# Kernel tuning notes

Hardware: AMD Instinct MI355X
Metric: run time of the kernel (lower is better)

## Reference

```python
import jax, jax.numpy as jnp
import numpy as np

ACT = jax.nn.leaky_relu  # Decima uses leaky_relu activations


def _mlp(x, params):
    # Linear + act chain (activation applied after every layer, incl. last, as in the torch code)
    for W, b in params:
        x = ACT(x @ W + b)
    return x


def setup_inputs() -> dict:
    key = jax.random.key(0)
    N, E, D = 500_000, 4_000_000, 8  # nodes, edges per depth, max_depth
    ks = jax.random.split(key, 32)
    inp = {}
    inp["inputs"] = jax.random.normal(ks[0], (N, 5), dtype=jnp.float32)
    inp["adj_src"] = jax.random.randint(ks[1], (D, E), 0, N, dtype=jnp.int32)
    inp["adj_dst"] = jax.random.randint(ks[2], (D, E), 0, N, dtype=jnp.int32)
    inp["masks"] = (jax.random.uniform(ks[3], (D, N, 1)) > 0.5).astype(jnp.float32)
    # MLP stacks: prep 5->16->32->8, proc/agg 8->16->32->8 (xavier-ish init, zero bias)
    dims = {"prep": [(5, 16), (16, 32), (32, 8)],
            "proc": [(8, 16), (16, 32), (32, 8)],
            "agg": [(8, 16), (16, 32), (32, 8)]}
    i = 4
    for name, ds in dims.items():
        for j, (a, b) in enumerate(ds):
            scale = np.sqrt(6.0 / (a + b)).astype(np.float32)
            inp[f"{name}_W{j}"] = jax.random.uniform(ks[i], (a, b), jnp.float32, -scale, scale)
            inp[f"{name}_b{j}"] = jnp.zeros((b,), jnp.float32)
            i += 1
    return inp


def reference(inputs, adj_src, adj_dst, masks,
              prep_W0, prep_b0, prep_W1, prep_b1, prep_W2, prep_b2,
              proc_W0, proc_b0, proc_W1, proc_b1, proc_W2, proc_b2,
              agg_W0, agg_b0, agg_W1, agg_b1, agg_W2, agg_b2):
    prep = [(prep_W0, prep_b0), (prep_W1, prep_b1), (prep_W2, prep_b2)]
    proc = [(proc_W0, proc_b0), (proc_W1, proc_b1), (proc_W2, proc_b2)]
    agg = [(agg_W0, agg_b0), (agg_W1, agg_b1), (agg_W2, agg_b2)]
    N = inputs.shape[0]
    max_depth = adj_src.shape[0]

    x = _mlp(inputs, prep)  # [N, 8]
    for d in range(max_depth):  # small fixed loop over depths
        y = _mlp(x, proc)  # [N, 8]
        # sparse adj matmul (unit-valued adjacency): out[i] = sum_{j: (i,j) in adj} y[j]
        y = jax.ops.segment_sum(y[adj_src[d]], adj_dst[d], num_segments=N)
        y = _mlp(y, agg)
        x = x + y * masks[d]  # mask + residual
    return x
```

## Files before the change

### kernel.cpp

```cpp
#include <hip/hip_runtime.h>
#include <hip/hip_fp16.h>


typedef unsigned long long u64;
typedef unsigned int u32;
typedef int v4i __attribute__((ext_vector_type(4)));

#define BKT_BITS 10
#define BKT_SIZE 1024
#define MAXNB    512
#define NBLK     256

template <int CH> struct Cfg;
template <> struct Cfg<4> { static const int CAPC = 6;  static const int SUBC = 24; };
template <> struct Cfg<2> { static const int CAPC = 14; static const int SUBC = 32; };
template <> struct Cfg<1> { static const int CAPC = 30; static const int SUBC = 64; };

__device__ __forceinline__ float lrelu(float v) { return fmaxf(v, 0.01f * v); }

template <int IN>
__device__ __forceinline__ void mlp3(const float* __restrict__ xin, float* __restrict__ yout,
    const float* __restrict__ sW0, const float* __restrict__ sb0,
    const float* __restrict__ sW1, const float* __restrict__ sb1,
    const float* __restrict__ sW2, const float* __restrict__ sb2)
{
    float h1[16];
#pragma unroll
    for (int o = 0; o < 16; ++o) {
        float s = sb0[o];
#pragma unroll
        for (int a = 0; a < IN; ++a) s = fmaf(xin[a], sW0[a * 16 + o], s);
        h1[o] = lrelu(s);
    }
    float h2[32];
#pragma unroll
    for (int o = 0; o < 32; ++o) {
        float s = sb1[o];
#pragma unroll
        for (int a = 0; a < 16; ++a) s = fmaf(h1[a], sW1[a * 32 + o], s);
        h2[o] = lrelu(s);
    }
#pragma unroll
    for (int o = 0; o < 8; ++o) {
        float s = sb2[o];
#pragma unroll
        for (int a = 0; a < 32; ++a) s = fmaf(h2[a], sW2[a * 8 + o], s);
        yout[o] = lrelu(s);
    }
}

__device__ __forceinline__ void ldw(float* d, const float* s, int n) {
    for (int t = threadIdx.x; t < n; t += 256) d[t] = s[t];
}

__device__ __forceinline__ uint4 pack_h8(const float* y) {
    __half2 p0 = __floats2half2_rn(y[0], y[1]);
    __half2 p1 = __floats2half2_rn(y[2], y[3]);
    __half2 p2 = __floats2half2_rn(y[4], y[5]);
    __half2 p3 = __floats2half2_rn(y[6], y[7]);
    uint4 v;
    v.x = *(u32*)&p0; v.y = *(u32*)&p1; v.z = *(u32*)&p2; v.w = *(u32*)&p3;
    return v;
}

__global__ __launch_bounds__(256) void prep_proc_kernel(
    const float* __restrict__ in, float* __restrict__ x, uint4* __restrict__ y,
    const float* pW0, const float* pb0, const float* pW1, const float* pb1,
    const float* pW2, const float* pb2,
    const float* cW0, const float* cb0, const float* cW1, const float* cb1,
    const float* cW2, const float* cb2, int N)
{
    __shared__ float P0[80],  Pb0[16], P1[512], Pb1[32], P2[256], Pb2[8];
    __shared__ float C0[128], Cb0[16], C1[512], Cb1[32], C2[256], Cb2[8];
    ldw(P0, pW0, 80);  ldw(Pb0, pb0, 16); ldw(P1, pW1, 512); ldw(Pb1, pb1, 32);
    ldw(P2, pW2, 256); ldw(Pb2, pb2, 8);
    ldw(C0, cW0, 128); ldw(Cb0, cb0, 16); ldw(C1, cW1, 512); ldw(Cb1, cb1, 32);
    ldw(C2, cW2, 256); ldw(Cb2, cb2, 8);
    __syncthreads();
    int i = blockIdx.x * 256 + threadIdx.x;
    if (i >= N) return;
    float xin[5];
#pragma unroll
    for (int k = 0; k < 5; ++k) xin[k] = in[(size_t)i * 5 + k];
    float xv[8];
    mlp3<5>(xin, xv, P0, Pb0, P1, Pb1, P2, Pb2);
    float4* xp = (float4*)(x + 8 * (size_t)i);
    xp[0] = make_float4(xv[0], xv[1], xv[2], xv[3]);
    xp[1] = make_float4(xv[4], xv[5], xv[6], xv[7]);
    float yv[8];
    mlp3<8>(xv, yv, C0, Cb0, C1, Cb1, C2, Cb2);
    y[i] = pack_h8(yv);
}

template <bool DO_PROC, int CHUNKS>
__global__ __launch_bounds__(256) void aggproc_kernel(
    const uint4* __restrict__ acc, float* __restrict__ x, const float* __restrict__ mask,
    uint4* __restrict__ y,
    const float* aW0, const float* ab0, const float* aW1, const float* ab1,
    const float* aW2, const float* ab2,
    const float* cW0, const float* cb0, const float* cW1, const float* cb1,
    const float* cW2, const float* cb2, int N)
{
    __shared__ float A0[128], Ab0[16], A1[512], Ab1[32], A2[256], Ab2[8];
    __shared__ float C0[128], Cb0[16], C1[512], Cb1[32], C2[256], Cb2[8];
    ldw(A0, aW0, 128); ldw(Ab0, ab0, 16); ldw(A1, aW1, 512); ldw(Ab1, ab1, 32);
    ldw(A2, aW2, 256); ldw(Ab2, ab2, 8);
    if (DO_PROC) {
        ldw(C0, cW0, 128); ldw(Cb0, cb0, 16); ldw(C1, cW1, 512); ldw(Cb1, cb1, 32);
        ldw(C2, cW2, 256); ldw(Cb2, cb2, 8);
    }
    __syncthreads();
    int i = blockIdx.x * 256 + threadIdx.x;
    if (i >= N) return;
    float ain[8] = {0.f, 0.f, 0.f, 0.f, 0.f, 0.f, 0.f, 0.f};
#pragma unroll
    for (int c = 0; c < CHUNKS; ++c) {
        uint4 v = acc[(size_t)c * N + i];
        float2 f0 = __half22float2(*(__half2*)&v.x);
        float2 f1 = __half22float2(*(__half2*)&v.y);
        float2 f2 = __half22float2(*(__half2*)&v.z);
        float2 f3 = __half22float2(*(__half2*)&v.w);
        ain[0] += f0.x; ain[1] += f0.y; ain[2] += f1.x; ain[3] += f1.y;
        ain[4] += f2.x; ain[5] += f2.y; ain[6] += f3.x; ain[7] += f3.y;
    }
    float ya[8];
    mlp3<8>(ain, ya, A0, Ab0, A1, Ab1, A2, Ab2);
    float m = mask[i];
    float4* xp = (float4*)(x + 8 * (size_t)i);
    float4 x0 = xp[0], x1 = xp[1];
    float xn[8] = {x0.x + ya[0] * m, x0.y + ya[1] * m, x0.z + ya[2] * m, x0.w + ya[3] * m,
                   x1.x + ya[4] * m, x1.y + ya[5] * m, x1.z + ya[6] * m, x1.w + ya[7] * m};
    xp[0] = make_float4(xn[0], xn[1], xn[2], xn[3]);
    xp[1] = make_float4(xn[4], xn[5], xn[6], xn[7]);
    if (DO_PROC) {
        float yv[8];
        mlp3<8>(xn, yv, C0, Cb0, C1, Cb1, C2, Cb2);
        y[i] = pack_h8(yv);
    }
}

__global__ __launch_bounds__(256) void mask_pack_kernel(
    const float* __restrict__ masks, u64* __restrict__ bitmaps, int N, int D, int BITW)
{
    int i = blockIdx.x * 256 + threadIdx.x;
    int lane = threadIdx.x & 63;
    for (int d = 0; d < D; ++d) {
        bool b = (i < N) ? (masks[(size_t)d * N + i] != 0.f) : false;
        u64 m = __ballot(b);
        if (lane == 0 && i < N) bitmaps[(size_t)d * BITW + (i >> 6)] = m;
    }
}

template <int CHUNKS>
__global__ __launch_bounds__(256) void place_kernel(
    const int* __restrict__ adj_src, const int* __restrict__ adj_dst,
    const u64* __restrict__ bitmaps,
    u32* __restrict__ ebuf_all,
    int* __restrict__ cnt_all,
    int E, int NB, int shift, int BITW, int Nhalf)
{
    constexpr int CAPC = Cfg<CHUNKS>::CAPC;
    constexpr int SUBC = Cfg<CHUNKS>::SUBC;
    const int dep = blockIdx.y;
    const int* src = adj_src + (size_t)dep * E;
    const int* dst = adj_dst + (size_t)dep * E;
    const u64* bitmap = bitmaps + (size_t)dep * BITW;
    u32* ebuf = ebuf_all + (size_t)dep * ((size_t)NB * CHUNKS * NBLK * SUBC);
    int* cnt_g = cnt_all + (size_t)dep * ((size_t)NB * CHUNKS * NBLK);

    __shared__ int lcnt[MAXNB * CHUNKS];
    __shared__ u32 stage[MAXNB * CHUNKS * CAPC];
    const int cells = NB * CHUNKS;
    for (int t = threadIdx.x; t < cells; t += 256) lcnt[t] = 0;
    __syncthreads();

    const int blk = blockIdx.x;
    const int E4 = E >> 2;
    const int CH4 = (E4 + NBLK - 1) / NBLK;
    const int base4 = blk * CH4;
    const int lim4 = min(base4 + CH4, E4);
    const v4i* src4 = (const v4i*)src;
    const v4i* dst4 = (const v4i*)dst;

#define PLACE(dv, sv) { int _d = (dv); \
    if (((_d < Nhalf) == (pass == 0)) && ((bitmap[_d >> 6] >> (_d & 63)) & 1ull)) { \
        int _cell = (_d >> BKT_BITS) * CHUNKS + ((u32)(sv) >> shift); \
        int _slot = atomicAdd(&lcnt[_cell], 1); \
        u32 _w = ((u32)(sv) << BKT_BITS) | (u32)(_d & (BKT_SIZE - 1)); \
        if (_slot < CAPC) stage[_cell * CAPC + _slot] = _w; \
        else if (_slot < SUBC) ebuf[((size_t)_cell * NBLK + blk) * SUBC + _slot] = _w; \
    } }

    for (int pass = 0; pass < 2; ++pass) {
        for (int i4 = base4 + threadIdx.x; i4 < lim4; i4 += 256) {
            v4i dv = __builtin_nontemporal_load(&dst4[i4]);
            v4i sv = __builtin_nontemporal_load(&src4[i4]);
            PLACE(dv.x, sv.x) PLACE(dv.y, sv.y) PLACE(dv.z, sv.z) PLACE(dv.w, sv.w)
        }
        if (blk == NBLK - 1)
            for (int e = (E4 << 2) + threadIdx.x; e < E; e += 256) { PLACE(dst[e], src[e]) }
    }
#undef PLACE

    __syncthreads();
    constexpr int SLOTW = (CAPC <= 8) ? 8 : (CAPC <= 16) ? 16 : 32;
    constexpr int CPW = 64 / SLOTW;
    int wave = threadIdx.x >> 6, lane = threadIdx.x & 63;
    int cslot = lane % SLOTW, coff = lane / SLOTW;
    for (int c0 = wave * CPW; c0 < cells; c0 += 4 * CPW) {
        int cell = c0 + coff;
        if (cell < cells) {
            int n = lcnt[cell];
            int ns = min(n, CAPC);
            size_t gb = ((size_t)cell * NBLK + blk) * SUBC;
            if (cslot < ns) ebuf[gb + cslot] = stage[cell * CAPC + cslot];
            if (cslot == 0) cnt_g[cell * NBLK + blk] = min(n, SUBC);
        }
    }
}

__device__ __forceinline__ void accum4(__half2* __restrict__ sacc, u32 w, uint4 v)
{
    int dl = (int)(w & (BKT_SIZE - 1));
    __half2* a = sacc + dl * 5;
    unsafeAtomicAdd(a + 0, *(__half2*)&v.x);
    unsafeAtomicAdd(a + 1, *(__half2*)&v.y);
    unsafeAtomicAdd(a + 2, *(__half2*)&v.z);
    unsafeAtomicAdd(a + 3, *(__half2*)&v.w);
}

template <int CHUNKS>
__global__ __launch_bounds__(256) void reduce_kernel(
    const uint4* __restrict__ y, const u32* __restrict__ ebuf, const int* __restrict__ cnt_g,
    uint4* __restrict__ acc, int N, int NB)
{
    constexpr int SUBC = Cfg<CHUNKS>::SUBC;
    int i = blockIdx.x, bucket, chunk;
    if (CHUNKS == 4)      { bucket = (i >> 3) * 2 + (i & 1); chunk = (i >> 1) & 3; }
    else if (CHUNKS == 2) { bucket = (i >> 3) * 4 + (i & 3); chunk = (i >> 2) & 1; }
    else                  { bucket = i; chunk = 0; }
    if (bucket >= NB) return;

    __shared__ __half2 sacc[BKT_SIZE * 5];
    for (int t = threadIdx.x; t < BKT_SIZE * 5; t += 256) ((u32*)sacc)[t] = 0u;
    __syncthreads();

    int cell = bucket * CHUNKS + chunk;
    int sb = cell * NBLK + threadIdx.x;
    int n = cnt_g[sb];
    const u32* r = ebuf + (size_t)sb * SUBC;

    int k = 0;
    for (; k + 3 < n; k += 4) {
        u32 w0 = r[k], w1 = r[k + 1], w2 = r[k + 2], w3 = r[k + 3];
        uint4 v0 = y[w0 >> BKT_BITS];
        uint4 v1 = y[w1 >> BKT_BITS];
        uint4 v2 = y[w2 >> BKT_BITS];
        uint4 v3 = y[w3 >> BKT_BITS];
        accum4(sacc, w0, v0);
        accum4(sacc, w1, v1);
        accum4(sacc, w2, v2);
        accum4(sacc, w3, v3);
    }
    for (; k < n; ++k) {
        u32 w = r[k];
        uint4 v = y[w >> BKT_BITS];
        accum4(sacc, w, v);
    }

    __syncthreads();
    int node0 = bucket << BKT_BITS;
    uint4* accc = acc + (size_t)chunk * N;
    for (int t = threadIdx.x; t < BKT_SIZE; t += 256) {
        int idx = node0 + t;
        if (idx < N) {
            __half2* a = sacc + t * 5;
            uint4 o;
            o.x = *(u32*)(a + 0); o.y = *(u32*)(a + 1);
            o.z = *(u32*)(a + 2); o.w = *(u32*)(a + 3);
            accc[idx] = o;
        }
    }
}

__global__ __launch_bounds__(256) void scatter_kernel(
    const uint4* __restrict__ y, const int* __restrict__ src, const int* __restrict__ dst,
    const float* __restrict__ mask, __half2* __restrict__ acc, int E)
{
    int e = blockIdx.x * blockDim.x + threadIdx.x;
    if (e >= E) return;
    int d = dst[e];
    if (mask[d] == 0.f) return;
    int s = src[e];
    uint4 v = y[s];
    __half2* o = acc + 4 * (size_t)d;
    unsafeAtomicAdd(o + 0, *(__half2*)&v.x);
    unsafeAtomicAdd(o + 1, *(__half2*)&v.y);
    unsafeAtomicAdd(o + 2, *(__half2*)&v.z);
    unsafeAtomicAdd(o + 3, *(__half2*)&v.w);
}

template <int CH>
static void run_fast(hipStream_t stream, bool batch, int N, int E, int D, int NB, int shift,
                     int BITW, int Nhalf, int nbN,
                     const int* adj_src, const int* adj_dst, const float* masks,
                     const u64* bitmaps, u32* ebuf, int* cnt_g,
                     uint4* y, uint4* acc, float* x,
                     const float* aW0, const float* ab0, const float* aW1, const float* ab1,
                     const float* aW2, const float* ab2,
                     const float* cW0, const float* cb0, const float* cW1, const float* cb1,
                     const float* cW2, const float* cb2)
{
    constexpr int SUBC = Cfg<CH>::SUBC;
    const size_t EB = (size_t)NB * CH * NBLK * SUBC;
    const size_t CN = (size_t)NB * CH * NBLK;
    const int rgrid = (CH == 4) ? ((NB + 1) / 2) * 8 : (CH == 2) ? ((NB + 3) / 4) * 8 : NB;

    if (batch)
        place_kernel<CH><<<dim3(NBLK, D), 256, 0, stream>>>(adj_src, adj_dst, bitmaps,
                                                            ebuf, cnt_g, E, NB, shift, BITW, Nhalf);

    for (int d = 0; d < D; ++d) {
        const float* mask_d = masks + (size_t)d * N;
        if (!batch)
            place_kernel<CH><<<dim3(NBLK, 1), 256, 0, stream>>>(
                adj_src + (size_t)d * E, adj_dst + (size_t)d * E, bitmaps + (size_t)d * BITW,
                ebuf, cnt_g, E, NB, shift, BITW, Nhalf);
        const u32* eb_d = ebuf + (batch ? (size_t)d * EB : 0);
        const int* cg_d = cnt_g + (batch ? (size_t)d * CN : 0);
        reduce_kernel<CH><<<rgrid, 256, 0, stream>>>(y, eb_d, cg_d, acc, N, NB);
        if (d < D - 1)
            aggproc_kernel<true, CH><<<nbN, 256, 0, stream>>>(acc, x, mask_d, y,
                aW0, ab0, aW1, ab1, aW2, ab2, cW0, cb0, cW1, cb1, cW2, cb2, N);
        else
            aggproc_kernel<false, CH><<<nbN, 256, 0, stream>>>(acc, x, mask_d, y,
                aW0, ab0, aW1, ab1, aW2, ab2, cW0, cb0, cW1, cb1, cW2, cb2, N);
    }
}

extern "C" void kernel_launch(void* const* d_in, const int* in_sizes, int n_in,
                              void* d_out, int out_size, void* d_ws, size_t ws_size,
                              hipStream_t stream)
{
    const float* inputs  = (const float*)d_in[0];
    const int*   adj_src = (const int*)d_in[1];
    const int*   adj_dst = (const int*)d_in[2];
    const float* masks   = (const float*)d_in[3];

    const float* pW0 = (const float*)d_in[4];  const float* pb0 = (const float*)d_in[5];
    const float* pW1 = (const float*)d_in[6];  const float* pb1 = (const float*)d_in[7];
    const float* pW2 = (const float*)d_in[8];  const float* pb2 = (const float*)d_in[9];
    const float* cW0 = (const float*)d_in[10]; const float* cb0 = (const float*)d_in[11];
    const float* cW1 = (const float*)d_in[12]; const float* cb1 = (const float*)d_in[13];
    const float* cW2 = (const float*)d_in[14]; const float* cb2 = (const float*)d_in[15];
    const float* aW0 = (const float*)d_in[16]; const float* ab0 = (const float*)d_in[17];
    const float* aW1 = (const float*)d_in[18]; const float* ab1 = (const float*)d_in[19];
    const float* aW2 = (const float*)d_in[20]; const float* ab2 = (const float*)d_in[21];

    const int N = in_sizes[0] / 5;
    const int D = in_sizes[3] / N;
    const int E = in_sizes[1] / D;
    const int NB = (N + BKT_SIZE - 1) >> BKT_BITS;
    const int BITW = (N + 63) >> 6;
    const int Nhalf = (BITW >> 1) << 6;

    float* x = (float*)d_out;

    auto layout_bytes = [&](int ch, bool batch) -> size_t {
        int subc = (ch == 4) ? 24 : (ch == 2) ? 32 : 64;
        int nd = batch ? D : 1;
        size_t s = 0;
        auto al = [&](size_t b) { s = (s + b + 255) & ~(size_t)255; };
        al((size_t)N * 16);
        al((size_t)ch * N * 16);
        al((size_t)D * BITW * 8);
        al((size_t)nd * NB * ch * NBLK * subc * 4);
        al((size_t)nd * NB * ch * NBLK * 4);
        return s;
    };
    int CHsel = 0; bool batch = false;
    if (NB <= MAXNB) {
        struct Opt { int ch; bool b; };
        const Opt opts[6] = {{4,true},{2,true},{1,true},{4,false},{2,false},{1,false}};
        for (int k = 0; k < 6; ++k)
            if (layout_bytes(opts[k].ch, opts[k].b) <= ws_size) { CHsel = opts[k].ch; batch = opts[k].b; break; }
    }
    bool fast = CHsel > 0;
    int subc = (CHsel == 4) ? 24 : (CHsel == 2) ? 32 : 64;
    int nd = batch ? D : 1;

    char* w = (char*)d_ws;
    size_t off = 0;
    auto take = [&](size_t bytes) { char* p = w + off; off = (off + bytes + 255) & ~(size_t)255; return p; };
    uint4* y   = (uint4*)take((size_t)N * 16);
    uint4* acc = (uint4*)take((size_t)(fast ? CHsel : 1) * N * 16);
    u64* bitmaps = (u64*)take((size_t)D * BITW * 8);
    u32* ebuf  = fast ? (u32*)take((size_t)nd * NB * CHsel * NBLK * subc * 4) : nullptr;
    int* cnt_g = fast ? (int*)take((size_t)nd * NB * CHsel * NBLK * 4) : nullptr;

    int shift = 0;
    if (fast) { while ((u32)(N - 1) >> shift >= (u32)CHsel) shift++; }

    const int BLK = 256;
    const int nbN = (N + BLK - 1) / BLK;
    const int nbE = (E + BLK - 1) / BLK;

    if (fast)
        mask_pack_kernel<<<nbN, BLK, 0, stream>>>(masks, bitmaps, N, D, BITW);

    prep_proc_kernel<<<nbN, BLK, 0, stream>>>(inputs, x, y,
                                              pW0, pb0, pW1, pb1, pW2, pb2,
                                              cW0, cb0, cW1, cb1, cW2, cb2, N);

    if (fast) {
        if (CHsel == 4)
            run_fast<4>(stream, batch, N, E, D, NB, shift, BITW, Nhalf, nbN, adj_src, adj_dst,
                        masks, bitmaps, ebuf, cnt_g, y, acc, x,
                        aW0, ab0, aW1, ab1, aW2, ab2, cW0, cb0, cW1, cb1, cW2, cb2);
        else if (CHsel == 2)
            run_fast<2>(stream, batch, N, E, D, NB, shift, BITW, Nhalf, nbN, adj_src, adj_dst,
                        masks, bitmaps, ebuf, cnt_g, y, acc, x,
                        aW0, ab0, aW1, ab1, aW2, ab2, cW0, cb0, cW1, cb1, cW2, cb2);
        else
            run_fast<1>(stream, batch, N, E, D, NB, shift, BITW, Nhalf, nbN, adj_src, adj_dst,
                        masks, bitmaps, ebuf, cnt_g, y, acc, x,
                        aW0, ab0, aW1, ab1, aW2, ab2, cW0, cb0, cW1, cb1, cW2, cb2);
    } else {
        for (int d = 0; d < D; ++d) {
            const float* mask_d = masks + (size_t)d * N;
            const int* src_d = adj_src + (size_t)d * E;
            const int* dst_d = adj_dst + (size_t)d * E;
            bool last = (d == D - 1);
            hipMemsetAsync(acc, 0, (size_t)N * 16, stream);
            scatter_kernel<<<nbE, BLK, 0, stream>>>(y, src_d, dst_d, mask_d, (__half2*)acc, E);
            if (!last)
                aggproc_kernel<true, 1><<<nbN, BLK, 0, stream>>>(acc, x, mask_d, y,
                    aW0, ab0, aW1, ab1, aW2, ab2, cW0, cb0, cW1, cb1, cW2, cb2, N);
            else
                aggproc_kernel<false, 1><<<nbN, BLK, 0, stream>>>(acc, x, mask_d, y,
                    aW0, ab0, aW1, ab1, aW2, ab2, cW0, cb0, cW1, cb1, cW2, cb2, N);
        }
    }
}
```

Baseline: 1.430 ms.

## Split place kernel halves across blocks and cache mask bitmap in LDS

The place kernel no longer loops twice over the edge list, once per destination half, inside one block. It launches a second grid dimension so separate blocks handle each half of the destination buckets. Each block copies its half of the mask bitmap into shared memory, replacing global bitmap lookups with LDS reads, and the CH=4 stage capacity grows from 6 to 8. This doubles the block count and halves per-block LDS for counters and staging. Each block still reads the whole edge chunk, so total edge traffic is unchanged, but the two halves can now run concurrently.

After: 1.354 ms. -5.3%, faster.

```diff
diff --git a/kernel.cpp b/kernel.cpp
--- a/kernel.cpp
+++ b/kernel.cpp
@@ -9,10 +9,11 @@
 #define BKT_BITS 10
 #define BKT_SIZE 1024
 #define MAXNB    512
+#define MAXNBH   256
 #define NBLK     256
 
 template <int CH> struct Cfg;
-template <> struct Cfg<4> { static const int CAPC = 6;  static const int SUBC = 24; };
+template <> struct Cfg<4> { static const int CAPC = 8;  static const int SUBC = 24; };
 template <> struct Cfg<2> { static const int CAPC = 14; static const int SUBC = 32; };
 template <> struct Cfg<1> { static const int CAPC = 30; static const int SUBC = 64; };
 
@@ -157,21 +158,30 @@
     const u64* __restrict__ bitmaps,
     u32* __restrict__ ebuf_all,
     int* __restrict__ cnt_all,
-    int E, int NB, int shift, int BITW, int Nhalf)
+    int E, int NB, int shift, int BITW, int NBH)
 {
     constexpr int CAPC = Cfg<CHUNKS>::CAPC;
     constexpr int SUBC = Cfg<CHUNKS>::SUBC;
-    const int dep = blockIdx.y;
+    const int dep = blockIdx.z;
+    const int half = blockIdx.y;
     const int* src = adj_src + (size_t)dep * E;
     const int* dst = adj_dst + (size_t)dep * E;
     const u64* bitmap = bitmaps + (size_t)dep * BITW;
     u32* ebuf = ebuf_all + (size_t)dep * ((size_t)NB * CHUNKS * NBLK * SUBC);
     int* cnt_g = cnt_all + (size_t)dep * ((size_t)NB * CHUNKS * NBLK);
 
-    __shared__ int lcnt[MAXNB * CHUNKS];
-    __shared__ u32 stage[MAXNB * CHUNKS * CAPC];
-    const int cells = NB * CHUNKS;
+    const int b_lo = half ? NBH : 0;
+    const int b_hi = half ? NB : NBH;
+    const int w_lo = b_lo << 4;
+    const int nw = min((b_hi - b_lo) << 4, BITW - w_lo);
+    const int Nsplit = NBH << BKT_BITS;
+
+    __shared__ int lcnt[MAXNBH * CHUNKS];
+    __shared__ u32 stage[MAXNBH * CHUNKS * CAPC];
+    __shared__ u64 sbm[MAXNBH * 16];
+    const int cells = (b_hi - b_lo) * CHUNKS;
     for (int t = threadIdx.x; t < cells; t += 256) lcnt[t] = 0;
+    for (int t = threadIdx.x; t < nw; t += 256) sbm[t] = bitmap[w_lo + t];
     __syncthreads();
 
     const int blk = blockIdx.x;
@@ -183,23 +193,22 @@
     const v4i* dst4 = (const v4i*)dst;
 
 #define PLACE(dv, sv) { int _d = (dv); \
-    if (((_d < Nhalf) == (pass == 0)) && ((bitmap[_d >> 6] >> (_d & 63)) & 1ull)) { \
-        int _cell = (_d >> BKT_BITS) * CHUNKS + ((u32)(sv) >> shift); \
-        int _slot = atomicAdd(&lcnt[_cell], 1); \
+    if ((int)(_d >= Nsplit) == half && ((sbm[(_d >> 6) - w_lo] >> (_d & 63)) & 1ull)) { \
+        int _lc = ((_d >> BKT_BITS) - b_lo) * CHUNKS + ((u32)(sv) >> shift); \
+        int _slot = atomicAdd(&lcnt[_lc], 1); \
         u32 _w = ((u32)(sv) << BKT_BITS) | (u32)(_d & (BKT_SIZE - 1)); \
-        if (_slot < CAPC) stage[_cell * CAPC + _slot] = _w; \
-        else if (_slot < SUBC) ebuf[((size_t)_cell * NBLK + blk) * SUBC + _slot] = _w; \
+        if (_slot < CAPC) stage[_lc * CAPC + _slot] = _w; \
+        else if (_slot < SUBC) \
+            ebuf[(((size_t)_lc + (size_t)b_lo * CHUNKS) * NBLK + blk) * SUBC + _slot] = _w; \
     } }
 
-    for (int pass = 0; pass < 2; ++pass) {
-        for (int i4 = base4 + threadIdx.x; i4 < lim4; i4 += 256) {
-            v4i dv = __builtin_nontemporal_load(&dst4[i4]);
-            v4i sv = __builtin_nontemporal_load(&src4[i4]);
-            PLACE(dv.x, sv.x) PLACE(dv.y, sv.y) PLACE(dv.z, sv.z) PLACE(dv.w, sv.w)
-        }
-        if (blk == NBLK - 1)
-            for (int e = (E4 << 2) + threadIdx.x; e < E; e += 256) { PLACE(dst[e], src[e]) }
-    }
+    for (int i4 = base4 + threadIdx.x; i4 < lim4; i4 += 256) {
+        v4i dv = __builtin_nontemporal_load(&dst4[i4]);
+        v4i sv = __builtin_nontemporal_load(&src4[i4]);
+        PLACE(dv.x, sv.x) PLACE(dv.y, sv.y) PLACE(dv.z, sv.z) PLACE(dv.w, sv.w)
+    }
+    if (blk == NBLK - 1)
+        for (int e = (E4 << 2) + threadIdx.x; e < E; e += 256) { PLACE(dst[e], src[e]) }
 #undef PLACE
 
     __syncthreads();
@@ -208,13 +217,14 @@
     int wave = threadIdx.x >> 6, lane = threadIdx.x & 63;
     int cslot = lane % SLOTW, coff = lane / SLOTW;
     for (int c0 = wave * CPW; c0 < cells; c0 += 4 * CPW) {
-        int cell = c0 + coff;
-        if (cell < cells) {
-            int n = lcnt[cell];
+        int lc = c0 + coff;
+        if (lc < cells) {
+            int n = lcnt[lc];
             int ns = min(n, CAPC);
-            size_t gb = ((size_t)cell * NBLK + blk) * SUBC;
-            if (cslot < ns) ebuf[gb + cslot] = stage[cell * CAPC + cslot];
-            if (cslot == 0) cnt_g[cell * NBLK + blk] = min(n, SUBC);
+            size_t gcell = (size_t)lc + (size_t)b_lo * CHUNKS;
+            size_t gb = (gcell * NBLK + blk) * SUBC;
+            if (cslot < ns) ebuf[gb + cslot] = stage[lc * CAPC + cslot];
+            if (cslot == 0) cnt_g[gcell * NBLK + blk] = min(n, SUBC);
         }
     }
 }
@@ -302,7 +312,7 @@
 
 template <int CH>
 static void run_fast(hipStream_t stream, bool batch, int N, int E, int D, int NB, int shift,
-                     int BITW, int Nhalf, int nbN,
+                     int BITW, int NBH, int nbN,
                      const int* adj_src, const int* adj_dst, const float* masks,
                      const u64* bitmaps, u32* ebuf, int* cnt_g,
                      uint4* y, uint4* acc, float* x,
@@ -317,15 +327,15 @@
     const int rgrid = (CH == 4) ? ((NB + 1) / 2) * 8 : (CH == 2) ? ((NB + 3) / 4) * 8 : NB;
 
     if (batch)
-        place_kernel<CH><<<dim3(NBLK, D), 256, 0, stream>>>(adj_src, adj_dst, bitmaps,
-                                                            ebuf, cnt_g, E, NB, shift, BITW, Nhalf);
+        place_kernel<CH><<<dim3(NBLK, 2, D), 256, 0, stream>>>(adj_src, adj_dst, bitmaps,
+                                                               ebuf, cnt_g, E, NB, shift, BITW, NBH);
 
     for (int d = 0; d < D; ++d) {
         const float* mask_d = masks + (size_t)d * N;
         if (!batch)
-            place_kernel<CH><<<dim3(NBLK, 1), 256, 0, stream>>>(
+            place_kernel<CH><<<dim3(NBLK, 2, 1), 256, 0, stream>>>(
                 adj_src + (size_t)d * E, adj_dst + (size_t)d * E, bitmaps + (size_t)d * BITW,
-                ebuf, cnt_g, E, NB, shift, BITW, Nhalf);
+                ebuf, cnt_g, E, NB, shift, BITW, NBH);
         const u32* eb_d = ebuf + (batch ? (size_t)d * EB : 0);
         const int* cg_d = cnt_g + (batch ? (size_t)d * CN : 0);
         reduce_kernel<CH><<<rgrid, 256, 0, stream>>>(y, eb_d, cg_d, acc, N, NB);
@@ -362,7 +372,7 @@
     const int E = in_sizes[1] / D;
     const int NB = (N + BKT_SIZE - 1) >> BKT_BITS;
     const int BITW = (N + 63) >> 6;
-    const int Nhalf = (BITW >> 1) << 6;
+    const int NBH = (NB + 1) / 2;
 
     float* x = (float*)d_out;
 
@@ -414,15 +424,15 @@
 
     if (fast) {
         if (CHsel == 4)
-            run_fast<4>(stream, batch, N, E, D, NB, shift, BITW, Nhalf, nbN, adj_src, adj_dst,
+            run_fast<4>(stream, batch, N, E, D, NB, shift, BITW, NBH, nbN, adj_src, adj_dst,
                         masks, bitmaps, ebuf, cnt_g, y, acc, x,
                         aW0, ab0, aW1, ab1, aW2, ab2, cW0, cb0, cW1, cb1, cW2, cb2);
         else if (CHsel == 2)
-            run_fast<2>(stream, batch, N, E, D, NB, shift, BITW, Nhalf, nbN, adj_src, adj_dst,
+            run_fast<2>(stream, batch, N, E, D, NB, shift, BITW, NBH, nbN, adj_src, adj_dst,
                         masks, bitmaps, ebuf, cnt_g, y, acc, x,
                         aW0, ab0, aW1, ab1, aW2, ab2, cW0, cb0, cW1, cb1, cW2, cb2);
         else
-            run_fast<1>(stream, batch, N, E, D, NB, shift, BITW, Nhalf, nbN, adj_src, adj_dst,
+            run_fast<1>(stream, batch, N, E, D, NB, shift, BITW, NBH, nbN, adj_src, adj_dst,
                         masks, bitmaps, ebuf, cnt_g, y, acc, x,
                         aW0, ab0, aW1, ab1, aW2, ab2, cW0, cb0, cW1, cb1, cW2, cb2);
     } else {
```
